# Kernel tuning notes

Measured on AMD Instinct MI355X. Metric: run time of the kernel, lower is better.

## Reference

```python
import jax, jax.numpy as jnp
import numpy as np

B, DIN, H = 16384, 512, 512
K = 7  # LC_i1, LC_i2, LC_f1, LC_f2, LC_o, LC_z (gate nets, idx 0..5), LC_d (decay net, idx 6)


def setup_inputs() -> dict:
    key = jax.random.key(0)
    ks = jax.random.split(key, 8)
    s1 = 1.0 / np.sqrt(DIN)
    s2 = 1.0 / np.sqrt(H)
    return {
        "hx": jax.random.normal(ks[0], (B, DIN), jnp.float32),
        "cx1": jax.random.normal(ks[1], (B, H), jnp.float32),
        "cx2": jax.random.normal(ks[2], (B, H), jnp.float32),
        # stacked params for the 7 sub-networks (same structure: Linear(DIN,H) -> Linear(H,H))
        "W1": jax.random.uniform(ks[3], (K, H, DIN), jnp.float32, -s1, s1),
        "b1": jax.random.uniform(ks[4], (K, H), jnp.float32, -s1, s1),
        "W2": jax.random.uniform(ks[5], (K, H, H), jnp.float32, -s2, s2),
        "b2": jax.random.uniform(ks[6], (K, H), jnp.float32, -s2, s2),
    }


def reference(hx, cx1, cx2, W1, b1, W2, b2):
    # layer 1 for all 7 nets at once: [K, B, H]
    h1 = jnp.einsum('bd,khd->kbh', hx, W1) + b1[:, None, :]
    # gate nets use tanh, decay net uses softplus
    a1 = jnp.concatenate([jnp.tanh(h1[:6]), jax.nn.softplus(h1[6:])], axis=0)
    # layer 2: [K, B, H]
    h2 = jnp.einsum('kbh,kgh->kbg', a1, W2) + b2[:, None, :]
    gates = jax.nn.sigmoid(jnp.tanh(h2[:6]))  # Gate_network: sigmoid(tanh(.))
    d = jax.nn.softplus(h2[6])                # Decay_network output (decay_coef, side state)
    i1, i2, f1, f2, o, zg = gates
    z = jnp.tanh(zg)                          # z = Tanh(LC_z(hx))
    cy1 = f1 * cx1 + i1 * z                   # side state self.cy1
    cy2 = f2 * cx2 + i2 * z
    return cy2
```

## Files before the change

kernel.cpp:

```cpp
#include <hip/hip_runtime.h>
#include <hip/hip_bf16.h>

typedef __attribute__((ext_vector_type(8))) __bf16 bf16x8;
typedef __attribute__((ext_vector_type(4))) __bf16 bf16x4;
typedef __attribute__((ext_vector_type(4))) float f32x4;

constexpr int M = 16384;
constexpr int K = 512;
constexpr int BK = 32;

__device__ __forceinline__ void async_copy16(const void* gsrc, void* ldst) {
  __builtin_amdgcn_global_load_lds(
      (const __attribute__((address_space(1))) unsigned int*)(gsrc),
      (__attribute__((address_space(3))) unsigned int*)(ldst),
      16, 0, 0);
}

__device__ __forceinline__ float frcp(float x) { return __builtin_amdgcn_rcpf(x); }
__device__ __forceinline__ float ftanh(float x) {
  return 1.0f - 2.0f * frcp(1.0f + __expf(2.0f * x));
}
__device__ __forceinline__ float fsigm(float x) {
  return frcp(1.0f + __expf(-x));
}

template <int LAYER>
__global__ __launch_bounds__(256) void gemm_kernel(
    const __bf16* __restrict__ A,
    const __bf16* __restrict__ W,
    const float* __restrict__ bias,
    __bf16* __restrict__ out)
{
  const int j = blockIdx.z;
  const int mbase = blockIdx.x * 128;
  const int nbase = blockIdx.y * 128;
  const __bf16* Aj = (LAYER == 2) ? (A + (size_t)j * M * K) : A;
  const __bf16* Wj = W + (size_t)j * K * K;

  __shared__ __align__(16) __bf16 smem[17408];

  const int tid  = threadIdx.x;
  const int wid  = tid >> 6;
  const int lane = tid & 63;
  const int wm   = (wid >> 1) * 64;
  const int wn   = (wid & 1) * 64;
  const int srow = wid * 16 + (lane >> 2);
  const int scol = ((lane & 3) ^ ((lane >> 3) & 3)) * 8;
  const int fr   = lane & 15;
  const int kc   = lane >> 4;
  const int sw   = (fr >> 1) & 3;
  const int rowq = kc * 4;

  auto stage = [&](int p, int k0) {
    __bf16* As = smem + p * 8192;
    __bf16* Bs = As + 4096;
#pragma unroll
    for (int r = 0; r < 2; ++r) {
      async_copy16(Aj + (size_t)(mbase + r * 64 + srow) * K + (k0 + scol),
                   (void*)&As[(r * 64 + wid * 16) * BK]);
      async_copy16(Wj + (size_t)(nbase + r * 64 + srow) * K + (k0 + scol),
                   (void*)&Bs[(r * 64 + wid * 16) * BK]);
    }
  };

  f32x4 acc[4][4] = {};

  stage(0, 0);
  int p = 0;
  for (int k0 = 0; k0 < K; k0 += BK) {
    __syncthreads();
    if (k0 + BK < K) stage(p ^ 1, k0 + BK);

    const __bf16* As = smem + p * 8192;
    const __bf16* Bs = As + 4096;
    bf16x8 af[4], bfr[4];
#pragma unroll
    for (int i = 0; i < 4; ++i) {
      af[i]  = *(const bf16x8*)&As[(wm + i * 16 + fr) * BK + ((kc ^ sw) * 8)];
      bfr[i] = *(const bf16x8*)&Bs[(wn + i * 16 + fr) * BK + ((kc ^ sw) * 8)];
    }
#pragma unroll
    for (int mi = 0; mi < 4; ++mi)
#pragma unroll
      for (int ni = 0; ni < 4; ++ni)
        acc[mi][ni] = __builtin_amdgcn_mfma_f32_16x16x32_bf16(
            af[mi], bfr[ni], acc[mi][ni], 0, 0, 0);
    p ^= 1;
  }

  float bv[4];
  const float* bj = bias + (2 * j + 1) * 512 + nbase + wn;
#pragma unroll
  for (int ni = 0; ni < 4; ++ni) bv[ni] = bj[ni * 16 + fr];

  __syncthreads();
#pragma unroll
  for (int mi = 0; mi < 4; ++mi)
#pragma unroll
    for (int ni = 0; ni < 4; ++ni)
#pragma unroll
      for (int r = 0; r < 4; ++r) {
        float v = acc[mi][ni][r] + bv[ni];
        float res;
        if constexpr (LAYER == 1) {
          res = ftanh(v);
        } else {
          res = (j == 2) ? ftanh(fsigm(ftanh(v))) : fsigm(ftanh(v));
        }
        smem[(wm + mi * 16 + rowq + r) * 136 + (wn + ni * 16 + fr)] =
            (__bf16)res;
      }
  __syncthreads();
#pragma unroll
  for (int it = 0; it < 8; ++it) {
    const int s = it * 256 + tid;
    const int row = s >> 4, ch = s & 15;
    bf16x8 v = *(const bf16x8*)&smem[row * 136 + ch * 8];
    *(bf16x8*)&out[(size_t)j * M * 512 + (size_t)(mbase + row) * 512 +
                   (nbase + ch * 8)] = v;
  }
}

__global__ __launch_bounds__(256) void final_kernel(
    const __bf16* __restrict__ gates, const float* __restrict__ cx2,
    float* __restrict__ out)
{
  constexpr size_t NH = (size_t)M * 512;
  const size_t i = ((size_t)blockIdx.x * 256 + threadIdx.x) * 8;
  bf16x8 i2 = *(const bf16x8*)&gates[i];
  bf16x8 f2 = *(const bf16x8*)&gates[NH + i];
  bf16x8 zz = *(const bf16x8*)&gates[2 * NH + i];
  f32x4 c0 = *(const f32x4*)&cx2[i];
  f32x4 c1 = *(const f32x4*)&cx2[i + 4];
#pragma unroll
  for (int h = 0; h < 2; ++h) {
    f32x4 r;
#pragma unroll
    for (int q = 0; q < 4; ++q) {
      const int e = h * 4 + q;
      r[q] = (float)f2[e] * (h ? c1[q] : c0[q]) + (float)i2[e] * (float)zz[e];
    }
    *(f32x4*)&out[i + h * 4] = r;
  }
}

__global__ __launch_bounds__(256) void cvt_hx(const float* __restrict__ src,
                                              __bf16* __restrict__ dst) {
  const size_t i = ((size_t)blockIdx.x * 256 + threadIdx.x) * 4;
  f32x4 v = *(const f32x4*)&src[i];
  *(bf16x4*)&dst[i] = __builtin_convertvector(v, bf16x4);
}

__global__ __launch_bounds__(256) void cvt_w(const float* __restrict__ src,
                                             __bf16* __restrict__ dst) {
  const int j = blockIdx.y;
  const size_t i = ((size_t)blockIdx.x * 256 + threadIdx.x) * 4;
  f32x4 v = *(const f32x4*)&src[(size_t)(2 * j + 1) * 262144 + i];
  *(bf16x4*)&dst[(size_t)j * 262144 + i] = __builtin_convertvector(v, bf16x4);
}

extern "C" void kernel_launch(void* const* d_in, const int* in_sizes, int n_in,
                              void* d_out, int out_size, void* d_ws, size_t ws_size,
                              hipStream_t stream) {
  const float* hx  = (const float*)d_in[0];
  const float* cx2 = (const float*)d_in[2];
  const float* W1  = (const float*)d_in[3];
  const float* b1  = (const float*)d_in[4];
  const float* W2  = (const float*)d_in[5];
  const float* b2  = (const float*)d_in[6];
  float* out = (float*)d_out;

  char* ws = (char*)d_ws;
  __bf16* hxb   = (__bf16*)(ws);
  __bf16* W1b   = (__bf16*)(ws + 16777216);
  __bf16* W2b   = (__bf16*)(ws + 18350080);
  __bf16* a1    = (__bf16*)(ws + 19922944);
  __bf16* gates = (__bf16*)(ws + 70254592);

  cvt_hx<<<8192, 256, 0, stream>>>(hx, hxb);
  cvt_w<<<dim3(256, 3), 256, 0, stream>>>(W1, W1b);
  cvt_w<<<dim3(256, 3), 256, 0, stream>>>(W2, W2b);

  gemm_kernel<1><<<dim3(128, 4, 3), 256, 0, stream>>>(hxb, W1b, b1, a1);
  gemm_kernel<2><<<dim3(128, 4, 3), 256, 0, stream>>>(a1, W2b, b2, gates);

  final_kernel<<<4096, 256, 0, stream>>>(gates, cx2, out);
}
```

Measured before the change: 233.4 us.

## Fuse both GEMM layers and final combine into one persistent row-block kernel

Replaces the separate hx conversion, two per-layer GEMM launches and the elementwise combine with a single kernel. Each block owns 64 rows, converts hx to bf16 on the fly, keeps the layer-1 activation in LDS, runs layer 2 from LDS, and holds the i2/f2 gates in registers until the z gate is computed and the output written. This removes the a1 and gates global round trips and several launches. In exchange each block must stream all weights itself, only 256 blocks are launched, and LDS use (about 136 KB) and register pressure are high, which limits occupancy.

Result: slower. 334.3 us (+43.2%).

```diff
diff --git a/kernel.cpp b/kernel.cpp
--- a/kernel.cpp
+++ b/kernel.cpp
@@ -5,9 +5,10 @@
 typedef __attribute__((ext_vector_type(4))) __bf16 bf16x4;
 typedef __attribute__((ext_vector_type(4))) float f32x4;
 
-constexpr int M = 16384;
-constexpr int K = 512;
+constexpr int M  = 16384;
+constexpr int K  = 512;
 constexpr int BK = 32;
+constexpr int R  = 64;
 
 __device__ __forceinline__ void async_copy16(const void* gsrc, void* ldst) {
   __builtin_amdgcn_global_load_lds(
@@ -20,143 +21,173 @@
 __device__ __forceinline__ float ftanh(float x) {
   return 1.0f - 2.0f * frcp(1.0f + __expf(2.0f * x));
 }
-__device__ __forceinline__ float fsigm(float x) {
-  return frcp(1.0f + __expf(-x));
-}
-
-template <int LAYER>
-__global__ __launch_bounds__(256) void gemm_kernel(
-    const __bf16* __restrict__ A,
-    const __bf16* __restrict__ W,
-    const float* __restrict__ bias,
-    __bf16* __restrict__ out)
+__device__ __forceinline__ float fsigm(float x) { return frcp(1.0f + __expf(-x)); }
+
+__global__ __launch_bounds__(512, 2) void fused_kernel(
+    const float* __restrict__ hx,
+    const __bf16* __restrict__ W1b,
+    const __bf16* __restrict__ W2b,
+    const float* __restrict__ b1,
+    const float* __restrict__ b2,
+    const float* __restrict__ cx2,
+    float* __restrict__ out)
 {
-  const int j = blockIdx.z;
-  const int mbase = blockIdx.x * 128;
-  const int nbase = blockIdx.y * 128;
-  const __bf16* Aj = (LAYER == 2) ? (A + (size_t)j * M * K) : A;
-  const __bf16* Wj = W + (size_t)j * K * K;
-
-  __shared__ __align__(16) __bf16 smem[17408];
-
-  const int tid  = threadIdx.x;
-  const int wid  = tid >> 6;
-  const int lane = tid & 63;
-  const int wm   = (wid >> 1) * 64;
-  const int wn   = (wid & 1) * 64;
+  __shared__ __align__(16) __bf16 smem[69632];
+  __bf16* const a1 = smem + 36864;
+
+  const int mbase = blockIdx.x * R;
+  const int tid = threadIdx.x, wid = tid >> 6, lane = tid & 63;
+  const int wn   = wid * 64;
   const int srow = wid * 16 + (lane >> 2);
   const int scol = ((lane & 3) ^ ((lane >> 3) & 3)) * 8;
-  const int fr   = lane & 15;
-  const int kc   = lane >> 4;
-  const int sw   = (fr >> 1) & 3;
-  const int rowq = kc * 4;
-
-  auto stage = [&](int p, int k0) {
-    __bf16* As = smem + p * 8192;
-    __bf16* Bs = As + 4096;
-#pragma unroll
-    for (int r = 0; r < 2; ++r) {
-      async_copy16(Aj + (size_t)(mbase + r * 64 + srow) * K + (k0 + scol),
-                   (void*)&As[(r * 64 + wid * 16) * BK]);
-      async_copy16(Wj + (size_t)(nbase + r * 64 + srow) * K + (k0 + scol),
-                   (void*)&Bs[(r * 64 + wid * 16) * BK]);
+  const int fr = lane & 15, kc = lane >> 4;
+  const int sw = (fr >> 1) & 3, rowq = kc * 4;
+
+  const int ar = tid >> 3, ac = tid & 7;
+  const int adst = ar * 32 + (((ac >> 1) ^ ((ar >> 1) & 3)) * 8) + (ac & 1) * 4;
+  const float* hxrow = hx + (size_t)(mbase + ar) * K + ac * 4;
+
+  bf16x4 i2s[4][4], f2s[4][4];
+
+  auto stageW = [&](int p, int k0, const __bf16* Wj) {
+#pragma unroll
+    for (int r = 0; r < 4; ++r)
+      async_copy16(Wj + (size_t)(r * 128 + srow) * K + (k0 + scol),
+                   (void*)&smem[p * 16384 + (r * 128 + wid * 16) * BK]);
+  };
+
+#pragma unroll 1
+  for (int j = 0; j < 3; ++j) {
+    const __bf16* WL1 = W1b + (size_t)j * 262144;
+    const __bf16* WL2 = W2b + (size_t)j * 262144;
+
+    {
+      f32x4 acc[4][4] = {};
+      {
+        f32x4 av = *(const f32x4*)(hxrow);
+        stageW(0, 0, WL1);
+        *(bf16x4*)&smem[32768 + adst] = __builtin_convertvector(av, bf16x4);
+      }
+      int p = 0;
+      for (int k0 = 0; k0 < K; k0 += BK) {
+        __syncthreads();
+        const bool pre = k0 + BK < K;
+        f32x4 av;
+        if (pre) {
+          av = *(const f32x4*)(hxrow + k0 + BK);
+          stageW(p ^ 1, k0 + BK, WL1);
+        }
+        bf16x8 af[4], bfr[4];
+#pragma unroll
+        for (int i = 0; i < 4; ++i) {
+          af[i]  = *(const bf16x8*)&smem[32768 + p * 2048 +
+                                         (i * 16 + fr) * BK + ((kc ^ sw) * 8)];
+          bfr[i] = *(const bf16x8*)&smem[p * 16384 +
+                                         (wn + i * 16 + fr) * BK + ((kc ^ sw) * 8)];
+        }
+#pragma unroll
+        for (int mi = 0; mi < 4; ++mi)
+#pragma unroll
+          for (int ni = 0; ni < 4; ++ni)
+            acc[mi][ni] = __builtin_amdgcn_mfma_f32_16x16x32_bf16(
+                af[mi], bfr[ni], acc[mi][ni], 0, 0, 0);
+        if (pre)
+          *(bf16x4*)&smem[32768 + (p ^ 1) * 2048 + adst] =
+              __builtin_convertvector(av, bf16x4);
+        p ^= 1;
+      }
+
+      const float* b1j = b1 + (2 * j + 1) * 512 + wn;
+      float bv[4];
+#pragma unroll
+      for (int ni = 0; ni < 4; ++ni) bv[ni] = b1j[ni * 16 + fr];
+#pragma unroll
+      for (int mi = 0; mi < 4; ++mi)
+#pragma unroll
+        for (int ni = 0; ni < 4; ++ni)
+#pragma unroll
+          for (int r = 0; r < 4; ++r) {
+            const int row = mi * 16 + rowq + r;
+            const int col = wn + ni * 16 + fr;
+            a1[(row * 512 + col) ^ ((row & 7) << 3)] =
+                (__bf16)ftanh(acc[mi][ni][r] + bv[ni]);
+          }
     }
-  };
-
-  f32x4 acc[4][4] = {};
-
-  stage(0, 0);
-  int p = 0;
-  for (int k0 = 0; k0 < K; k0 += BK) {
-    __syncthreads();
-    if (k0 + BK < K) stage(p ^ 1, k0 + BK);
-
-    const __bf16* As = smem + p * 8192;
-    const __bf16* Bs = As + 4096;
-    bf16x8 af[4], bfr[4];
-#pragma unroll
-    for (int i = 0; i < 4; ++i) {
-      af[i]  = *(const bf16x8*)&As[(wm + i * 16 + fr) * BK + ((kc ^ sw) * 8)];
-      bfr[i] = *(const bf16x8*)&Bs[(wn + i * 16 + fr) * BK + ((kc ^ sw) * 8)];
+
+    {
+      stageW(0, 0, WL2);
+      f32x4 acc[4][4] = {};
+      int p = 0;
+      for (int k0 = 0; k0 < K; k0 += BK) {
+        __syncthreads();
+        if (k0 + BK < K) stageW(p ^ 1, k0 + BK, WL2);
+        bf16x8 af[4], bfr[4];
+#pragma unroll
+        for (int i = 0; i < 4; ++i) {
+          const int row = i * 16 + fr;
+          af[i]  = *(const bf16x8*)&a1[(row * 512 + k0 + kc * 8) ^
+                                       ((row & 7) << 3)];
+          bfr[i] = *(const bf16x8*)&smem[p * 16384 +
+                                         (wn + i * 16 + fr) * BK + ((kc ^ sw) * 8)];
+        }
+#pragma unroll
+        for (int mi = 0; mi < 4; ++mi)
+#pragma unroll
+          for (int ni = 0; ni < 4; ++ni)
+            acc[mi][ni] = __builtin_amdgcn_mfma_f32_16x16x32_bf16(
+                af[mi], bfr[ni], acc[mi][ni], 0, 0, 0);
+        p ^= 1;
+      }
+
+      const float* b2j = b2 + (2 * j + 1) * 512 + wn;
+      float bv[4];
+#pragma unroll
+      for (int ni = 0; ni < 4; ++ni) bv[ni] = b2j[ni * 16 + fr];
+      if (j == 0) {
+#pragma unroll
+        for (int mi = 0; mi < 4; ++mi)
+#pragma unroll
+          for (int ni = 0; ni < 4; ++ni)
+#pragma unroll
+            for (int r = 0; r < 4; ++r)
+              i2s[mi][ni][r] = (__bf16)fsigm(ftanh(acc[mi][ni][r] + bv[ni]));
+      } else if (j == 1) {
+#pragma unroll
+        for (int mi = 0; mi < 4; ++mi)
+#pragma unroll
+          for (int ni = 0; ni < 4; ++ni)
+#pragma unroll
+            for (int r = 0; r < 4; ++r)
+              f2s[mi][ni][r] = (__bf16)fsigm(ftanh(acc[mi][ni][r] + bv[ni]));
+      } else {
+#pragma unroll
+        for (int mi = 0; mi < 4; ++mi)
+#pragma unroll
+          for (int ni = 0; ni < 4; ++ni)
+#pragma unroll
+            for (int r = 0; r < 4; ++r) {
+              const __bf16 zb =
+                  (__bf16)ftanh(fsigm(ftanh(acc[mi][ni][r] + bv[ni])));
+              const size_t idx = (size_t)(mbase + mi * 16 + rowq + r) * 512 +
+                                 (wn + ni * 16 + fr);
+              out[idx] = (float)f2s[mi][ni][r] * cx2[idx] +
+                         (float)i2s[mi][ni][r] * (float)zb;
+            }
+      }
     }
-#pragma unroll
-    for (int mi = 0; mi < 4; ++mi)
-#pragma unroll
-      for (int ni = 0; ni < 4; ++ni)
-        acc[mi][ni] = __builtin_amdgcn_mfma_f32_16x16x32_bf16(
-            af[mi], bfr[ni], acc[mi][ni], 0, 0, 0);
-    p ^= 1;
   }
-
-  float bv[4];
-  const float* bj = bias + (2 * j + 1) * 512 + nbase + wn;
-#pragma unroll
-  for (int ni = 0; ni < 4; ++ni) bv[ni] = bj[ni * 16 + fr];
-
-  __syncthreads();
-#pragma unroll
-  for (int mi = 0; mi < 4; ++mi)
-#pragma unroll
-    for (int ni = 0; ni < 4; ++ni)
-#pragma unroll
-      for (int r = 0; r < 4; ++r) {
-        float v = acc[mi][ni][r] + bv[ni];
-        float res;
-        if constexpr (LAYER == 1) {
-          res = ftanh(v);
-        } else {
-          res = (j == 2) ? ftanh(fsigm(ftanh(v))) : fsigm(ftanh(v));
-        }
-        smem[(wm + mi * 16 + rowq + r) * 136 + (wn + ni * 16 + fr)] =
-            (__bf16)res;
-      }
-  __syncthreads();
-#pragma unroll
-  for (int it = 0; it < 8; ++it) {
-    const int s = it * 256 + tid;
-    const int row = s >> 4, ch = s & 15;
-    bf16x8 v = *(const bf16x8*)&smem[row * 136 + ch * 8];
-    *(bf16x8*)&out[(size_t)j * M * 512 + (size_t)(mbase + row) * 512 +
-                   (nbase + ch * 8)] = v;
-  }
-}
-
-__global__ __launch_bounds__(256) void final_kernel(
-    const __bf16* __restrict__ gates, const float* __restrict__ cx2,
-    float* __restrict__ out)
-{
-  constexpr size_t NH = (size_t)M * 512;
-  const size_t i = ((size_t)blockIdx.x * 256 + threadIdx.x) * 8;
-  bf16x8 i2 = *(const bf16x8*)&gates[i];
-  bf16x8 f2 = *(const bf16x8*)&gates[NH + i];
-  bf16x8 zz = *(const bf16x8*)&gates[2 * NH + i];
-  f32x4 c0 = *(const f32x4*)&cx2[i];
-  f32x4 c1 = *(const f32x4*)&cx2[i + 4];
-#pragma unroll
-  for (int h = 0; h < 2; ++h) {
-    f32x4 r;
-#pragma unroll
-    for (int q = 0; q < 4; ++q) {
-      const int e = h * 4 + q;
-      r[q] = (float)f2[e] * (h ? c1[q] : c0[q]) + (float)i2[e] * (float)zz[e];
-    }
-    *(f32x4*)&out[i + h * 4] = r;
-  }
-}
-
-__global__ __launch_bounds__(256) void cvt_hx(const float* __restrict__ src,
+}
+
+__global__ __launch_bounds__(256) void cvt_w6(const float* __restrict__ W1,
+                                              const float* __restrict__ W2,
                                               __bf16* __restrict__ dst) {
+  const int y = blockIdx.y;
+  const float* src = (y < 3) ? W1 + (size_t)(2 * y + 1) * 262144
+                             : W2 + (size_t)(2 * (y - 3) + 1) * 262144;
+  __bf16* d = dst + (size_t)y * 262144;
   const size_t i = ((size_t)blockIdx.x * 256 + threadIdx.x) * 4;
   f32x4 v = *(const f32x4*)&src[i];
-  *(bf16x4*)&dst[i] = __builtin_convertvector(v, bf16x4);
-}
-
-__global__ __launch_bounds__(256) void cvt_w(const float* __restrict__ src,
-                                             __bf16* __restrict__ dst) {
-  const int j = blockIdx.y;
-  const size_t i = ((size_t)blockIdx.x * 256 + threadIdx.x) * 4;
-  f32x4 v = *(const f32x4*)&src[(size_t)(2 * j + 1) * 262144 + i];
-  *(bf16x4*)&dst[(size_t)j * 262144 + i] = __builtin_convertvector(v, bf16x4);
+  *(bf16x4*)&d[i] = __builtin_convertvector(v, bf16x4);
 }
 
 extern "C" void kernel_launch(void* const* d_in, const int* in_sizes, int n_in,
@@ -168,21 +199,11 @@
   const float* b1  = (const float*)d_in[4];
   const float* W2  = (const float*)d_in[5];
   const float* b2  = (const float*)d_in[6];
-  float* out = (float*)d_out;
-
-  char* ws = (char*)d_ws;
-  __bf16* hxb   = (__bf16*)(ws);
-  __bf16* W1b   = (__bf16*)(ws + 16777216);
-  __bf16* W2b   = (__bf16*)(ws + 18350080);
-  __bf16* a1    = (__bf16*)(ws + 19922944);
-  __bf16* gates = (__bf16*)(ws + 70254592);
-
-  cvt_hx<<<8192, 256, 0, stream>>>(hx, hxb);
-  cvt_w<<<dim3(256, 3), 256, 0, stream>>>(W1, W1b);
-  cvt_w<<<dim3(256, 3), 256, 0, stream>>>(W2, W2b);
-
-  gemm_kernel<1><<<dim3(128, 4, 3), 256, 0, stream>>>(hxb, W1b, b1, a1);
-  gemm_kernel<2><<<dim3(128, 4, 3), 256, 0, stream>>>(a1, W2b, b2, gates);
-
-  final_kernel<<<4096, 256, 0, stream>>>(gates, cx2, out);
-}
+
+  __bf16* W1b = (__bf16*)d_ws;
+  __bf16* W2b = W1b + 3 * 262144;
+
+  cvt_w6<<<dim3(256, 6), 256, 0, stream>>>(W1, W2, W1b);
+  fused_kernel<<<256, 512, 0, stream>>>(hx, W1b, W2b, b1, b2, cx2,
+                                        (float*)d_out);
+}
```

## Fuse fp32 hx conversion into layer-1 GEMM and final combine into z-GEMM epilogue

Applied to the files above, without the earlier changes.

Layer-1 GEMM now reads fp32 hx directly, converts it to bf16 and stores it into swizzled LDS, so the separate hx conversion pass and its bf16 buffer are gone. The z-gate GEMM runs as its own launch whose epilogue reads the i2/f2 gates and cx2 and writes the final fp32 output, replacing the standalone elementwise kernel. The two weight-conversion launches merge into one. The costs are synchronous fp32 global loads in the layer-1 staging path instead of async LDS copies, an uncoalesced per-element epilogue in mode 3, and a third layer-2 launch that is only a third as wide.

Result: slower. 271.5 us (+16.3%).

```diff
diff --git a/kernel.cpp b/kernel.cpp
--- a/kernel.cpp
+++ b/kernel.cpp
@@ -20,22 +20,28 @@
 __device__ __forceinline__ float ftanh(float x) {
   return 1.0f - 2.0f * frcp(1.0f + __expf(2.0f * x));
 }
-__device__ __forceinline__ float fsigm(float x) {
-  return frcp(1.0f + __expf(-x));
-}
+__device__ __forceinline__ float fsigm(float x) { return frcp(1.0f + __expf(-x)); }
 
-template <int LAYER>
+template <int MODE>
 __global__ __launch_bounds__(256) void gemm_kernel(
-    const __bf16* __restrict__ A,
+    const float* __restrict__ hx,
+    const __bf16* __restrict__ Ab,
     const __bf16* __restrict__ W,
     const float* __restrict__ bias,
-    __bf16* __restrict__ out)
+    __bf16* __restrict__ outb,
+    const __bf16* __restrict__ gates,
+    const float* __restrict__ cx2,
+    float* __restrict__ outf)
 {
   const int j = blockIdx.z;
+  const int jj = (MODE == 3) ? 2 : j;
   const int mbase = blockIdx.x * 128;
   const int nbase = blockIdx.y * 128;
-  const __bf16* Aj = (LAYER == 2) ? (A + (size_t)j * M * K) : A;
-  const __bf16* Wj = W + (size_t)j * K * K;
+  constexpr size_t NH = (size_t)M * 512;
+
+  const __bf16* Wj = W + (size_t)jj * 262144;
+  const __bf16* Abj = (MODE >= 2) ? Ab + (size_t)jj * NH : nullptr;
+  const int brow = 2 * jj + 1;
 
   __shared__ __align__(16) __bf16 smem[17408];
 
@@ -51,15 +57,35 @@
   const int sw   = (fr >> 1) & 3;
   const int rowq = kc * 4;
 
+  const int ar = tid >> 1;
+  const int cb = (tid & 1) * 2;
+  const int asw = (ar >> 1) & 3;
+  const float* hxrow =
+      (MODE == 1) ? hx + (size_t)(mbase + ar) * K + cb * 8 : nullptr;
+
   auto stage = [&](int p, int k0) {
     __bf16* As = smem + p * 8192;
     __bf16* Bs = As + 4096;
 #pragma unroll
-    for (int r = 0; r < 2; ++r) {
-      async_copy16(Aj + (size_t)(mbase + r * 64 + srow) * K + (k0 + scol),
-                   (void*)&As[(r * 64 + wid * 16) * BK]);
+    for (int r = 0; r < 2; ++r)
       async_copy16(Wj + (size_t)(nbase + r * 64 + srow) * K + (k0 + scol),
                    (void*)&Bs[(r * 64 + wid * 16) * BK]);
+    if constexpr (MODE >= 2) {
+#pragma unroll
+      for (int r = 0; r < 2; ++r)
+        async_copy16(Abj + (size_t)(mbase + r * 64 + srow) * K + (k0 + scol),
+                     (void*)&As[(r * 64 + wid * 16) * BK]);
+    } else {
+      const float* hp = hxrow + k0;
+      f32x4 v0 = *(const f32x4*)(hp);
+      f32x4 v1 = *(const f32x4*)(hp + 4);
+      f32x4 v2 = *(const f32x4*)(hp + 8);
+      f32x4 v3 = *(const f32x4*)(hp + 12);
+      __bf16* As_ = As + ar * 32;
+      *(bf16x4*)&As_[(cb ^ asw) * 8]           = __builtin_convertvector(v0, bf16x4);
+      *(bf16x4*)&As_[(cb ^ asw) * 8 + 4]       = __builtin_convertvector(v1, bf16x4);
+      *(bf16x4*)&As_[((cb + 1) ^ asw) * 8]     = __builtin_convertvector(v2, bf16x4);
+      *(bf16x4*)&As_[((cb + 1) ^ asw) * 8 + 4] = __builtin_convertvector(v3, bf16x4);
     }
   };
 
@@ -89,74 +115,60 @@
   }
 
   float bv[4];
-  const float* bj = bias + (2 * j + 1) * 512 + nbase + wn;
+  const float* bj = bias + (size_t)brow * 512 + nbase + wn;
 #pragma unroll
   for (int ni = 0; ni < 4; ++ni) bv[ni] = bj[ni * 16 + fr];
 
-  __syncthreads();
+  if constexpr (MODE <= 2) {
+    __syncthreads();
 #pragma unroll
-  for (int mi = 0; mi < 4; ++mi)
+    for (int mi = 0; mi < 4; ++mi)
 #pragma unroll
-    for (int ni = 0; ni < 4; ++ni)
+      for (int ni = 0; ni < 4; ++ni)
 #pragma unroll
-      for (int r = 0; r < 4; ++r) {
-        float v = acc[mi][ni][r] + bv[ni];
-        float res;
-        if constexpr (LAYER == 1) {
-          res = ftanh(v);
-        } else {
-          res = (j == 2) ? ftanh(fsigm(ftanh(v))) : fsigm(ftanh(v));
+        for (int r = 0; r < 4; ++r) {
+          float v = acc[mi][ni][r] + bv[ni];
+          float res = (MODE == 1) ? ftanh(v) : fsigm(ftanh(v));
+          smem[(wm + mi * 16 + rowq + r) * 136 + (wn + ni * 16 + fr)] =
+              (__bf16)res;
         }
-        smem[(wm + mi * 16 + rowq + r) * 136 + (wn + ni * 16 + fr)] =
-            (__bf16)res;
-      }
-  __syncthreads();
+    __syncthreads();
 #pragma unroll
-  for (int it = 0; it < 8; ++it) {
-    const int s = it * 256 + tid;
-    const int row = s >> 4, ch = s & 15;
-    bf16x8 v = *(const bf16x8*)&smem[row * 136 + ch * 8];
-    *(bf16x8*)&out[(size_t)j * M * 512 + (size_t)(mbase + row) * 512 +
-                   (nbase + ch * 8)] = v;
+    for (int it = 0; it < 8; ++it) {
+      const int s = it * 256 + tid;
+      const int row = s >> 4, ch = s & 15;
+      bf16x8 v = *(const bf16x8*)&smem[row * 136 + ch * 8];
+      *(bf16x8*)&outb[(size_t)j * NH + (size_t)(mbase + row) * 512 +
+                      (nbase + ch * 8)] = v;
+    }
+  } else {
+#pragma unroll
+    for (int mi = 0; mi < 4; ++mi)
+#pragma unroll
+      for (int ni = 0; ni < 4; ++ni)
+#pragma unroll
+        for (int r = 0; r < 4; ++r) {
+          float v = acc[mi][ni][r] + bv[ni];
+          const __bf16 zb = (__bf16)ftanh(fsigm(ftanh(v)));
+          const size_t idx =
+              (size_t)(mbase + wm + mi * 16 + rowq + r) * 512 +
+              (nbase + wn + ni * 16 + fr);
+          outf[idx] = (float)gates[NH + idx] * cx2[idx] +
+                      (float)gates[idx] * (float)zb;
+        }
   }
 }
 
-__global__ __launch_bounds__(256) void final_kernel(
-    const __bf16* __restrict__ gates, const float* __restrict__ cx2,
-    float* __restrict__ out)
-{
-  constexpr size_t NH = (size_t)M * 512;
-  const size_t i = ((size_t)blockIdx.x * 256 + threadIdx.x) * 8;
-  bf16x8 i2 = *(const bf16x8*)&gates[i];
-  bf16x8 f2 = *(const bf16x8*)&gates[NH + i];
-  bf16x8 zz = *(const bf16x8*)&gates[2 * NH + i];
-  f32x4 c0 = *(const f32x4*)&cx2[i];
-  f32x4 c1 = *(const f32x4*)&cx2[i + 4];
-#pragma unroll
-  for (int h = 0; h < 2; ++h) {
-    f32x4 r;
-#pragma unroll
-    for (int q = 0; q < 4; ++q) {
-      const int e = h * 4 + q;
-      r[q] = (float)f2[e] * (h ? c1[q] : c0[q]) + (float)i2[e] * (float)zz[e];
-    }
-    *(f32x4*)&out[i + h * 4] = r;
-  }
-}
-
-__global__ __launch_bounds__(256) void cvt_hx(const float* __restrict__ src,
+__global__ __launch_bounds__(256) void cvt_w6(const float* __restrict__ W1,
+                                              const float* __restrict__ W2,
                                               __bf16* __restrict__ dst) {
+  const int y = blockIdx.y;
+  const float* src = (y < 3) ? W1 + (size_t)(2 * y + 1) * 262144
+                             : W2 + (size_t)(2 * (y - 3) + 1) * 262144;
+  __bf16* d = dst + (size_t)y * 262144;
   const size_t i = ((size_t)blockIdx.x * 256 + threadIdx.x) * 4;
   f32x4 v = *(const f32x4*)&src[i];
-  *(bf16x4*)&dst[i] = __builtin_convertvector(v, bf16x4);
-}
-
-__global__ __launch_bounds__(256) void cvt_w(const float* __restrict__ src,
-                                             __bf16* __restrict__ dst) {
-  const int j = blockIdx.y;
-  const size_t i = ((size_t)blockIdx.x * 256 + threadIdx.x) * 4;
-  f32x4 v = *(const f32x4*)&src[(size_t)(2 * j + 1) * 262144 + i];
-  *(bf16x4*)&dst[(size_t)j * 262144 + i] = __builtin_convertvector(v, bf16x4);
+  *(bf16x4*)&d[i] = __builtin_convertvector(v, bf16x4);
 }
 
 extern "C" void kernel_launch(void* const* d_in, const int* in_sizes, int n_in,
@@ -171,18 +183,17 @@
   float* out = (float*)d_out;
 
   char* ws = (char*)d_ws;
-  __bf16* hxb   = (__bf16*)(ws);
-  __bf16* W1b   = (__bf16*)(ws + 16777216);
-  __bf16* W2b   = (__bf16*)(ws + 18350080);
-  __bf16* a1    = (__bf16*)(ws + 19922944);
-  __bf16* gates = (__bf16*)(ws + 70254592);
+  __bf16* W1b   = (__bf16*)(ws);
+  __bf16* W2b   = (__bf16*)(ws + 1572864);
+  __bf16* a1    = (__bf16*)(ws + 3145728);
+  __bf16* gates = (__bf16*)(ws + 53477376);
 
-  cvt_hx<<<8192, 256, 0, stream>>>(hx, hxb);
-  cvt_w<<<dim3(256, 3), 256, 0, stream>>>(W1, W1b);
-  cvt_w<<<dim3(256, 3), 256, 0, stream>>>(W2, W2b);
+  cvt_w6<<<dim3(256, 6), 256, 0, stream>>>(W1, W2, W1b);
 
-  gemm_kernel<1><<<dim3(128, 4, 3), 256, 0, stream>>>(hxb, W1b, b1, a1);
-  gemm_kernel<2><<<dim3(128, 4, 3), 256, 0, stream>>>(a1, W2b, b2, gates);
-
-  final_kernel<<<4096, 256, 0, stream>>>(gates, cx2, out);
+  gemm_kernel<1><<<dim3(128, 4, 3), 256, 0, stream>>>(
+      hx, nullptr, W1b, b1, a1, nullptr, nullptr, nullptr);
+  gemm_kernel<2><<<dim3(128, 4, 2), 256, 0, stream>>>(
+      nullptr, a1, W2b, b2, gates, nullptr, nullptr, nullptr);
+  gemm_kernel<3><<<dim3(128, 4, 1), 256, 0, stream>>>(
+      nullptr, a1, W2b, b2, nullptr, gates, cx2, out);
 }
```
